# Performance work log

Measured on AMD Instinct MI355X. Metric: run time of the kernel, lower is better.

Reference implementation:

```python
import jax, jax.numpy as jnp
import numpy as np

N, E, D, L, G = 50000, 800000, 96, 3, 256
CD, CH, LAT = 7, 5, 64
BN_EPS = 1e-5


def setup_inputs() -> dict:
    key = jax.random.key(0)
    ks = iter(jax.random.split(key, 32))
    nrm = lambda shape, s=0.1: jax.random.normal(next(ks), shape, dtype=jnp.float32) * s
    return {
        "x": jax.random.normal(next(ks), (N, D), dtype=jnp.float32),
        "cond": jax.random.normal(next(ks), (G, CD), dtype=jnp.float32),
        "edge_index": jax.random.randint(next(ks), (2, E), 0, N),
        "batch": jnp.sort(jax.random.randint(next(ks), (N,), 0, G)),
        "conv_W1": nrm((L, D, D)),
        "conv_b1": nrm((L, D)),
        "conv_g": jnp.ones((L, D), jnp.float32),
        "conv_beta": jnp.zeros((L, D), jnp.float32),
        "conv_mean": jnp.zeros((L, D), jnp.float32),
        "conv_var": jnp.ones((L, D), jnp.float32),
        "conv_W2": nrm((L, D, D)),
        "conv_b2": nrm((L, D)),
        "cW1": nrm((CD, CH)),
        "cb1": nrm((CH,)),
        "cg": jnp.ones((CH,), jnp.float32),
        "cbeta": jnp.zeros((CH,), jnp.float32),
        "cmean": jnp.zeros((CH,), jnp.float32),
        "cvar": jnp.ones((CH,), jnp.float32),
        "cW2": nrm((CH, CH)),
        "cb2": nrm((CH,)),
        "bn_g": jnp.ones((D + CH,), jnp.float32),
        "bn_b": jnp.zeros((D + CH,), jnp.float32),
        "bn_mean": jnp.zeros((D + CH,), jnp.float32),
        "bn_var": jnp.ones((D + CH,), jnp.float32),
        "fc_W": nrm((D + CH, LAT)),
        "fc_b": nrm((LAT,)),
    }


def _bn(h, g, b, mu, var):
    # BatchNorm1d in eval mode: normalize with running stats
    return (h - mu) * (g / jnp.sqrt(var + BN_EPS)) + b


def reference(x, cond, edge_index, batch,
              conv_W1, conv_b1, conv_g, conv_beta, conv_mean, conv_var, conv_W2, conv_b2,
              cW1, cb1, cg, cbeta, cmean, cvar, cW2, cb2,
              bn_g, bn_b, bn_mean, bn_var, fc_W, fc_b):
    src, dst = edge_index[0], edge_index[1]
    n_nodes = x.shape[0]
    h = x
    for l in range(conv_W1.shape[0]):
        # GINConv (eps=0): h_i <- MLP(h_i + sum_{j in N(i)} h_j)
        agg = jax.ops.segment_sum(h[src], dst, num_segments=n_nodes)  # [N, D]
        h = h + agg
        h = jax.nn.leaky_relu(h @ conv_W1[l] + conv_b1[l], 0.2)
        h = _bn(h, conv_g[l], conv_beta[l], conv_mean[l], conv_var[l])
        h = jax.nn.leaky_relu(h @ conv_W2[l] + conv_b2[l], 0.2)
        # dropout is identity in eval mode
    pooled = jax.ops.segment_sum(h, batch, num_segments=cond.shape[0])  # [G, D]
    # conditioning MLP: Linear -> BN -> ReLU -> Linear -> ReLU
    c = cond @ cW1 + cb1
    c = jax.nn.relu(_bn(c, cg, cbeta, cmean, cvar))
    c = jax.nn.relu(c @ cW2 + cb2)
    out = jnp.concatenate([c, pooled], axis=1)  # [G, CH + D]
    out = _bn(out, bn_g, bn_b, bn_mean, bn_var)
    return out @ fc_W + fc_b  # [G, LAT]
```

## Files before the change

### kernel.cpp

```cpp
#include <hip/hip_runtime.h>

#define BN_EPS 1e-5f

__device__ __forceinline__ float lrelu(float x){ return x > 0.f ? x : 0.2f*x; }

struct F3 { float x, y, z; };


__global__ __launch_bounds__(256) void hist_k(const int* __restrict__ dst,
                                              int* __restrict__ deg, int E){
  int e = blockIdx.x*256 + threadIdx.x;
  if (e < E) atomicAdd(&deg[dst[e]], 1);
}

__global__ __launch_bounds__(256) void scan1_k(int* __restrict__ degoff,
                                               int* __restrict__ bsum, int N){
  __shared__ int s[256];
  int t = threadIdx.x, i = blockIdx.x*256 + t;
  int v = (i < N) ? degoff[i] : 0;
  s[t] = v; __syncthreads();
  int x = v;
  for (int d = 1; d < 256; d <<= 1){
    int y = (t >= d) ? s[t-d] : 0;
    __syncthreads();
    x += y; s[t] = x;
    __syncthreads();
  }
  if (i < N) degoff[i] = x - v;
  if (t == 255) bsum[blockIdx.x] = x;
}

__global__ __launch_bounds__(256) void scan2_k(int* __restrict__ bsum, int nb){
  __shared__ int s[256];
  int t = threadIdx.x;
  int v = (t < nb) ? bsum[t] : 0;
  s[t] = v; __syncthreads();
  int x = v;
  for (int d = 1; d < 256; d <<= 1){
    int y = (t >= d) ? s[t-d] : 0;
    __syncthreads();
    x += y; s[t] = x;
    __syncthreads();
  }
  if (t < nb) bsum[t] = x - v;
}

__global__ __launch_bounds__(256) void scan3_k(int* __restrict__ off,
                                               int* __restrict__ cursor,
                                               const int* __restrict__ bsum,
                                               int N, int E){
  int i = blockIdx.x*256 + threadIdx.x;
  if (i < N){
    int o = off[i] + bsum[blockIdx.x];
    off[i] = o; cursor[i] = o;
  }
  if (i == 0) off[N] = E;
}

__global__ __launch_bounds__(256) void scatter_k(const int* __restrict__ src,
                                                 const int* __restrict__ dst,
                                                 int* __restrict__ cursor,
                                                 int* __restrict__ srcs, int E){
  int e = blockIdx.x*256 + threadIdx.x;
  if (e < E){
    int p = atomicAdd(&cursor[dst[e]], 1);
    srcs[p] = src[e];
  }
}

__global__ __launch_bounds__(256) void agg_k(const float* __restrict__ hin,
                                             float* __restrict__ hout,
                                             const int* __restrict__ off,
                                             const int* __restrict__ srcs, int N){
  int node = blockIdx.x*8 + (threadIdx.x >> 5);
  int ln = threadIdx.x & 31;
  if (node >= N) return;
  F3 a = *((const F3*)(hin + (size_t)node*96) + ln);
  float bx = 0.f, by = 0.f, bz = 0.f;
  int jb = off[node], je = off[node+1];
  int j = jb;
  for (; j+1 < je; j += 2){
    int s0 = srcs[j], s1 = srcs[j+1];
    F3 q0 = *((const F3*)(hin + (size_t)s0*96) + ln);
    F3 q1 = *((const F3*)(hin + (size_t)s1*96) + ln);
    a.x += q0.x; a.y += q0.y; a.z += q0.z;
    bx  += q1.x; by  += q1.y; bz  += q1.z;
  }
  if (j < je){
    int s0 = srcs[j];
    F3 q0 = *((const F3*)(hin + (size_t)s0*96) + ln);
    a.x += q0.x; a.y += q0.y; a.z += q0.z;
  }
  a.x += bx; a.y += by; a.z += bz;
  *((F3*)(hout + (size_t)node*96) + ln) = a;
}

__global__ __launch_bounds__(256) void mlp_sw_k(
    const float* __restrict__ hin, float* __restrict__ hout,
    const float* __restrict__ W1, const float* __restrict__ b1,
    const float* __restrict__ g, const float* __restrict__ beta,
    const float* __restrict__ mean, const float* __restrict__ var,
    const float* __restrict__ W2, const float* __restrict__ b2, int N)
{
  __shared__ float hT[96*67];
  int t = threadIdx.x;
  int nbase = blockIdx.x * 64;
  int lim = (N - nbase) * 96;
  const float* hbase = hin + (size_t)nbase*96;

  #pragma unroll
  for (int i = 0; i < 24; ++i){
    int tid = t + 256*i;
    float v = (tid < lim) ? hbase[tid] : 0.f;
    int n = tid / 96, k = tid - n*96;
    hT[k*67 + n] = v;
  }
  __syncthreads();

  int ln = t & 63;
  int d0 = __builtin_amdgcn_readfirstlane((t >> 6) * 24);

  float acc[24];
  #pragma unroll
  for (int j = 0; j < 24; ++j) acc[j] = b1[d0+j];
  #pragma unroll 2
  for (int k = 0; k < 96; ++k){
    float hk = hT[k*67 + ln];
    const float* wr = W1 + k*96 + d0;
    #pragma unroll
    for (int j = 0; j < 24; ++j) acc[j] = fmaf(hk, wr[j], acc[j]);
  }
  __syncthreads();

  #pragma unroll
  for (int j = 0; j < 24; ++j){
    int d = d0 + j;
    float s = g[d] * rsqrtf(var[d] + BN_EPS);
    float m = lrelu(acc[j]);
    hT[d*67 + ln] = (m - mean[d])*s + beta[d];
  }
  __syncthreads();

  #pragma unroll
  for (int j = 0; j < 24; ++j) acc[j] = b2[d0+j];
  #pragma unroll 2
  for (int k = 0; k < 96; ++k){
    float hk = hT[k*67 + ln];
    const float* wr = W2 + k*96 + d0;
    #pragma unroll
    for (int j = 0; j < 24; ++j) acc[j] = fmaf(hk, wr[j], acc[j]);
  }
  __syncthreads();

  #pragma unroll
  for (int j = 0; j < 24; ++j)
    hT[(d0+j)*67 + ln] = lrelu(acc[j]);
  __syncthreads();

  float* obase = hout + (size_t)nbase*96;
  #pragma unroll
  for (int i = 0; i < 24; ++i){
    int tid = t + 256*i;
    int n = tid / 96, k = tid - n*96;
    if (tid < lim) obase[tid] = hT[k*67 + n];
  }
}


__global__ __launch_bounds__(256) void bounds_k(const int* __restrict__ batch,
                                                int* __restrict__ go, int N, int G){
  int i = blockIdx.x*256 + threadIdx.x;
  if (i >= N) return;
  int b = batch[i];
  int prev = (i == 0) ? -1 : batch[i-1];
  for (int g = prev+1; g <= b; ++g) go[g] = i;
  if (i == N-1){
    for (int g = b+1; g <= G; ++g) go[g] = N;
  }
}

__global__ __launch_bounds__(384) void poolfinal_k(
    const float* __restrict__ h, const int* __restrict__ go,
    const float* __restrict__ cond,
    const float* __restrict__ cW1, const float* __restrict__ cb1,
    const float* __restrict__ cg, const float* __restrict__ cbeta,
    const float* __restrict__ cmean, const float* __restrict__ cvar,
    const float* __restrict__ cW2, const float* __restrict__ cb2,
    const float* __restrict__ bn_g, const float* __restrict__ bn_b,
    const float* __restrict__ bn_mean, const float* __restrict__ bn_var,
    const float* __restrict__ fcW, const float* __restrict__ fcb,
    float* __restrict__ out)
{
  __shared__ float ps[4][96];
  __shared__ float pl[96];
  int g = blockIdx.x, t = threadIdx.x;
  int s = t / 96, d = t - s*96;
  {
    float acc = 0.f;
    int nb = go[g], ne = go[g+1];
    for (int n = nb + s; n < ne; n += 4) acc += h[(size_t)n*96 + d];
    ps[s][d] = acc;
  }
  __syncthreads();
  if (t < 96) pl[t] = ps[0][t] + ps[1][t] + ps[2][t] + ps[3][t];
  __syncthreads();

  if (t < 64){
    float cin[7];
    #pragma unroll
    for (int j = 0; j < 7; ++j) cin[j] = cond[g*7+j];
    float c1[5];
    #pragma unroll
    for (int i = 0; i < 5; ++i){
      float a = cb1[i];
      #pragma unroll
      for (int j = 0; j < 7; ++j) a = fmaf(cin[j], cW1[j*5+i], a);
      float sc = cg[i] * rsqrtf(cvar[i] + BN_EPS);
      a = (a - cmean[i])*sc + cbeta[i];
      c1[i] = a > 0.f ? a : 0.f;
    }
    float c2[5];
    #pragma unroll
    for (int i = 0; i < 5; ++i){
      float a = cb2[i];
      #pragma unroll
      for (int j = 0; j < 5; ++j) a = fmaf(c1[j], cW2[j*5+i], a);
      c2[i] = a > 0.f ? a : 0.f;
    }
    float acc = fcb[t];
    #pragma unroll
    for (int j = 0; j < 5; ++j){
      float sc = bn_g[j] * rsqrtf(bn_var[j] + BN_EPS);
      float nb = (c2[j] - bn_mean[j])*sc + bn_b[j];
      acc = fmaf(nb, fcW[j*64 + t], acc);
    }
    for (int j = 5; j < 101; ++j){
      float vj = pl[j-5];
      float sc = bn_g[j] * rsqrtf(bn_var[j] + BN_EPS);
      float nb = (vj - bn_mean[j])*sc + bn_b[j];
      acc = fmaf(nb, fcW[j*64 + t], acc);
    }
    out[g*64 + t] = acc;
  }
}


extern "C" void kernel_launch(void* const* d_in, const int* in_sizes, int n_in,
                              void* d_out, int out_size, void* d_ws, size_t ws_size,
                              hipStream_t stream)
{
  const float* x         = (const float*)d_in[0];
  const float* cond      = (const float*)d_in[1];
  const int*   ei        = (const int*)  d_in[2];
  const int*   batch     = (const int*)  d_in[3];
  const float* conv_W1   = (const float*)d_in[4];
  const float* conv_b1   = (const float*)d_in[5];
  const float* conv_g    = (const float*)d_in[6];
  const float* conv_beta = (const float*)d_in[7];
  const float* conv_mean = (const float*)d_in[8];
  const float* conv_var  = (const float*)d_in[9];
  const float* conv_W2   = (const float*)d_in[10];
  const float* conv_b2   = (const float*)d_in[11];
  const float* cW1       = (const float*)d_in[12];
  const float* cb1       = (const float*)d_in[13];
  const float* cg        = (const float*)d_in[14];
  const float* cbeta     = (const float*)d_in[15];
  const float* cmean     = (const float*)d_in[16];
  const float* cvar      = (const float*)d_in[17];
  const float* cW2       = (const float*)d_in[18];
  const float* cb2       = (const float*)d_in[19];
  const float* bn_g      = (const float*)d_in[20];
  const float* bn_b      = (const float*)d_in[21];
  const float* bn_mean   = (const float*)d_in[22];
  const float* bn_var    = (const float*)d_in[23];
  const float* fc_W      = (const float*)d_in[24];
  const float* fc_b      = (const float*)d_in[25];

  const int D = 96;
  int N = in_sizes[0] / D;
  int G = in_sizes[1] / 7;
  int E = in_sizes[2] / 2;
  const int* src = ei;
  const int* dst = ei + E;

  char* p = (char*)d_ws;
  auto carve = [&](size_t bytes)->void*{
    void* r = (void*)p; p += (bytes + 255) & ~(size_t)255; return r;
  };
  int*   off    = (int*)  carve((size_t)(N+1)*4);
  int*   cursor = (int*)  carve((size_t)N*4);
  int*   bsum   = (int*)  carve(256*4);
  int*   srcs   = (int*)  carve((size_t)E*4);
  int*   go     = (int*)  carve((size_t)(G+1)*4);
  float* hA     = (float*)carve((size_t)N*D*4);
  float* hB     = (float*)carve((size_t)N*D*4);

  int gE = (E+255)/256, gN = (N+255)/256;

  hipMemsetAsync(off, 0, (size_t)(N+1)*4, stream);
  hist_k   <<<gE, 256, 0, stream>>>(dst, off, E);
  scan1_k  <<<gN, 256, 0, stream>>>(off, bsum, N);
  scan2_k  <<<1,  256, 0, stream>>>(bsum, gN);
  scan3_k  <<<gN, 256, 0, stream>>>(off, cursor, bsum, N, E);
  scatter_k<<<gE, 256, 0, stream>>>(src, dst, cursor, srcs, E);
  bounds_k <<<gN, 256, 0, stream>>>(batch, go, N, G);

  const float* hin = x;
  int nblk = (N+63)/64;
  for (int l = 0; l < 3; ++l){
    agg_k<<<(N+7)/8, 256, 0, stream>>>(hin, hB, off, srcs, N);
    mlp_sw_k<<<nblk, 256, 0, stream>>>(hB, hA,
        conv_W1 + (size_t)l*D*D, conv_b1 + l*D,
        conv_g + l*D, conv_beta + l*D, conv_mean + l*D, conv_var + l*D,
        conv_W2 + (size_t)l*D*D, conv_b2 + l*D, N);
    hin = hA;
  }

  poolfinal_k<<<G, 384, 0, stream>>>(hA, go, cond,
                                     cW1, cb1, cg, cbeta, cmean, cvar,
                                     cW2, cb2, bn_g, bn_b, bn_mean, bn_var,
                                     fc_W, fc_b, (float*)d_out);
}
```

Before: 486.6 us.

## Two-level bucketed CSR build and 512-thread MLP blocks

Replaces the single global-atomic scatter that builds the CSR source list with a two-pass bucket partition. Edges are first grouped into 128-node buckets using shared-memory histograms, then scattered per bucket with LDS atomics, which is meant to cut contended global atomics and random writes. It adds an 8-byte-per-edge intermediate buffer and several extra launches. Separately, the MLP kernel now runs 512 threads per block, each computing 12 output columns instead of 24, with k-chunked register staging of the LDS reads; this lowers register pressure and raises parallelism per block.

```diff
diff --git a/kernel.cpp b/kernel.cpp
--- a/kernel.cpp
+++ b/kernel.cpp
@@ -46,25 +46,98 @@
 }
 
 __global__ __launch_bounds__(256) void scan3_k(int* __restrict__ off,
-                                               int* __restrict__ cursor,
                                                const int* __restrict__ bsum,
                                                int N, int E){
   int i = blockIdx.x*256 + threadIdx.x;
-  if (i < N){
-    int o = off[i] + bsum[blockIdx.x];
-    off[i] = o; cursor[i] = o;
-  }
+  if (i < N) off[i] += bsum[blockIdx.x];
   if (i == 0) off[N] = E;
 }
 
-__global__ __launch_bounds__(256) void scatter_k(const int* __restrict__ src,
-                                                 const int* __restrict__ dst,
-                                                 int* __restrict__ cursor,
-                                                 int* __restrict__ srcs, int E){
-  int e = blockIdx.x*256 + threadIdx.x;
-  if (e < E){
-    int p = atomicAdd(&cursor[dst[e]], 1);
-    srcs[p] = src[e];
+#define EB 4096
+
+__global__ __launch_bounds__(256) void bhist_k(const int* __restrict__ dst,
+                                               int* __restrict__ bcnt, int E){
+  __shared__ int bh[512];
+  int t = threadIdx.x;
+  bh[t] = 0; bh[t+256] = 0;
+  __syncthreads();
+  int e0 = blockIdx.x*EB;
+  for (int i = 0; i < EB/256; ++i){
+    int e = e0 + i*256 + t;
+    if (e < E) atomicAdd(&bh[dst[e] >> 7], 1);
+  }
+  __syncthreads();
+  if (bh[t])     atomicAdd(&bcnt[t],     bh[t]);
+  if (bh[t+256]) atomicAdd(&bcnt[t+256], bh[t+256]);
+}
+
+__global__ __launch_bounds__(512) void bscan_k(const int* __restrict__ bcnt,
+                                               int* __restrict__ bkt_off,
+                                               int* __restrict__ gcur, int E){
+  __shared__ int s[512];
+  int t = threadIdx.x;
+  int v = bcnt[t];
+  s[t] = v; __syncthreads();
+  int x = v;
+  for (int d = 1; d < 512; d <<= 1){
+    int y = (t >= d) ? s[t-d] : 0;
+    __syncthreads();
+    x += y; s[t] = x;
+    __syncthreads();
+  }
+  bkt_off[t] = x - v;
+  gcur[t]    = x - v;
+  if (t == 511) bkt_off[512] = E;
+}
+
+__global__ __launch_bounds__(256) void bpart_k(const int* __restrict__ src,
+                                               const int* __restrict__ dst,
+                                               int* __restrict__ gcur,
+                                               int2* __restrict__ ebuf, int E){
+  __shared__ int bh[512];
+  __shared__ int base[512];
+  int t = threadIdx.x;
+  bh[t] = 0; bh[t+256] = 0;
+  __syncthreads();
+  int e0 = blockIdx.x*EB;
+  for (int i = 0; i < EB/256; ++i){
+    int e = e0 + i*256 + t;
+    if (e < E) atomicAdd(&bh[dst[e] >> 7], 1);
+  }
+  __syncthreads();
+  #pragma unroll
+  for (int h = 0; h < 2; ++h){
+    int b = t + h*256;
+    base[b] = bh[b] ? atomicAdd(&gcur[b], bh[b]) : 0;
+  }
+  __syncthreads();
+  for (int i = 0; i < EB/256; ++i){
+    int e = e0 + i*256 + t;
+    if (e < E){
+      int s = src[e], d = dst[e];
+      int p = atomicAdd(&base[d >> 7], 1);
+      ebuf[p] = make_int2(s, d);
+    }
+  }
+}
+
+__global__ __launch_bounds__(256) void bscat_k(const int2* __restrict__ ebuf,
+                                               const int* __restrict__ bkt_off,
+                                               const int* __restrict__ off,
+                                               int* __restrict__ srcs, int N){
+  __shared__ int lcur[128];
+  int b = blockIdx.x, t = threadIdx.x;
+  int node_lo = b << 7;
+  if (t < 128){
+    int n = node_lo + t;
+    lcur[t] = (n < N) ? off[n] : 0;
+  }
+  __syncthreads();
+  int eb = bkt_off[b], ee = bkt_off[b+1];
+  for (int e = eb + t; e < ee; e += 256){
+    int2 sd = ebuf[e];
+    int p = atomicAdd(&lcur[sd.y - node_lo], 1);
+    srcs[p] = sd.x;
   }
 }
 
@@ -95,7 +168,7 @@
   *((F3*)(hout + (size_t)node*96) + ln) = a;
 }
 
-__global__ __launch_bounds__(256) void mlp_sw_k(
+__global__ __launch_bounds__(512) void mlp_sw_k(
     const float* __restrict__ hin, float* __restrict__ hout,
     const float* __restrict__ W1, const float* __restrict__ b1,
     const float* __restrict__ g, const float* __restrict__ beta,
@@ -109,8 +182,8 @@
   const float* hbase = hin + (size_t)nbase*96;
 
   #pragma unroll
-  for (int i = 0; i < 24; ++i){
-    int tid = t + 256*i;
+  for (int i = 0; i < 12; ++i){
+    int tid = t + 512*i;
     float v = (tid < lim) ? hbase[tid] : 0.f;
     int n = tid / 96, k = tid - n*96;
     hT[k*67 + n] = v;
@@ -118,22 +191,26 @@
   __syncthreads();
 
   int ln = t & 63;
-  int d0 = __builtin_amdgcn_readfirstlane((t >> 6) * 24);
-
-  float acc[24];
-  #pragma unroll
-  for (int j = 0; j < 24; ++j) acc[j] = b1[d0+j];
-  #pragma unroll 2
-  for (int k = 0; k < 96; ++k){
-    float hk = hT[k*67 + ln];
-    const float* wr = W1 + k*96 + d0;
-    #pragma unroll
-    for (int j = 0; j < 24; ++j) acc[j] = fmaf(hk, wr[j], acc[j]);
-  }
-  __syncthreads();
-
-  #pragma unroll
-  for (int j = 0; j < 24; ++j){
+  int d0 = __builtin_amdgcn_readfirstlane((t >> 6) * 12);
+
+  float acc[12];
+  #pragma unroll
+  for (int j = 0; j < 12; ++j) acc[j] = b1[d0+j];
+  for (int kc = 0; kc < 96; kc += 8){
+    float hc[8];
+    #pragma unroll
+    for (int i = 0; i < 8; ++i) hc[i] = hT[(kc+i)*67 + ln];
+    #pragma unroll
+    for (int i = 0; i < 8; ++i){
+      const float* wr = W1 + (kc+i)*96 + d0;
+      #pragma unroll
+      for (int j = 0; j < 12; ++j) acc[j] = fmaf(hc[i], wr[j], acc[j]);
+    }
+  }
+  __syncthreads();
+
+  #pragma unroll
+  for (int j = 0; j < 12; ++j){
     int d = d0 + j;
     float s = g[d] * rsqrtf(var[d] + BN_EPS);
     float m = lrelu(acc[j]);
@@ -142,25 +219,29 @@
   __syncthreads();
 
   #pragma unroll
-  for (int j = 0; j < 24; ++j) acc[j] = b2[d0+j];
-  #pragma unroll 2
-  for (int k = 0; k < 96; ++k){
-    float hk = hT[k*67 + ln];
-    const float* wr = W2 + k*96 + d0;
-    #pragma unroll
-    for (int j = 0; j < 24; ++j) acc[j] = fmaf(hk, wr[j], acc[j]);
-  }
-  __syncthreads();
-
-  #pragma unroll
-  for (int j = 0; j < 24; ++j)
+  for (int j = 0; j < 12; ++j) acc[j] = b2[d0+j];
+  for (int kc = 0; kc < 96; kc += 8){
+    float hc[8];
+    #pragma unroll
+    for (int i = 0; i < 8; ++i) hc[i] = hT[(kc+i)*67 + ln];
+    #pragma unroll
+    for (int i = 0; i < 8; ++i){
+      const float* wr = W2 + (kc+i)*96 + d0;
+      #pragma unroll
+      for (int j = 0; j < 12; ++j) acc[j] = fmaf(hc[i], wr[j], acc[j]);
+    }
+  }
+  __syncthreads();
+
+  #pragma unroll
+  for (int j = 0; j < 12; ++j)
     hT[(d0+j)*67 + ln] = lrelu(acc[j]);
   __syncthreads();
 
   float* obase = hout + (size_t)nbase*96;
   #pragma unroll
-  for (int i = 0; i < 24; ++i){
-    int tid = t + 256*i;
+  for (int i = 0; i < 12; ++i){
+    int tid = t + 512*i;
     int n = tid / 96, k = tid - n*96;
     if (tid < lim) obase[tid] = hT[k*67 + n];
   }
@@ -287,29 +368,36 @@
   auto carve = [&](size_t bytes)->void*{
     void* r = (void*)p; p += (bytes + 255) & ~(size_t)255; return r;
   };
-  int*   off    = (int*)  carve((size_t)(N+1)*4);
-  int*   cursor = (int*)  carve((size_t)N*4);
-  int*   bsum   = (int*)  carve(256*4);
-  int*   srcs   = (int*)  carve((size_t)E*4);
-  int*   go     = (int*)  carve((size_t)(G+1)*4);
-  float* hA     = (float*)carve((size_t)N*D*4);
-  float* hB     = (float*)carve((size_t)N*D*4);
-
-  int gE = (E+255)/256, gN = (N+255)/256;
-
-  hipMemsetAsync(off, 0, (size_t)(N+1)*4, stream);
-  hist_k   <<<gE, 256, 0, stream>>>(dst, off, E);
-  scan1_k  <<<gN, 256, 0, stream>>>(off, bsum, N);
-  scan2_k  <<<1,  256, 0, stream>>>(bsum, gN);
-  scan3_k  <<<gN, 256, 0, stream>>>(off, cursor, bsum, N, E);
-  scatter_k<<<gE, 256, 0, stream>>>(src, dst, cursor, srcs, E);
-  bounds_k <<<gN, 256, 0, stream>>>(batch, go, N, G);
+  int*   off     = (int*)  carve((size_t)(N+1)*4);
+  int*   bsum    = (int*)  carve(256*4);
+  int*   bcnt    = (int*)  carve(512*4);
+  int*   bkt_off = (int*)  carve(513*4);
+  int*   gcur    = (int*)  carve(512*4);
+  int2*  ebuf    = (int2*) carve((size_t)E*8);
+  int*   srcs    = (int*)  carve((size_t)E*4);
+  int*   go      = (int*)  carve((size_t)(G+1)*4);
+  float* hA      = (float*)carve((size_t)N*D*4);
+  float* hB      = (float*)carve((size_t)N*D*4);
+
+  int gE = (E+255)/256, gN = (N+255)/256, gEB = (E+EB-1)/EB;
+
+  hipMemsetAsync(off,  0, (size_t)(N+1)*4, stream);
+  hipMemsetAsync(bcnt, 0, 512*4, stream);
+  hist_k <<<gE, 256, 0, stream>>>(dst, off, E);
+  scan1_k<<<gN, 256, 0, stream>>>(off, bsum, N);
+  scan2_k<<<1,  256, 0, stream>>>(bsum, gN);
+  scan3_k<<<gN, 256, 0, stream>>>(off, bsum, N, E);
+  bhist_k<<<gEB, 256, 0, stream>>>(dst, bcnt, E);
+  bscan_k<<<1,  512, 0, stream>>>(bcnt, bkt_off, gcur, E);
+  bpart_k<<<gEB, 256, 0, stream>>>(src, dst, gcur, ebuf, E);
+  bscat_k<<<512, 256, 0, stream>>>(ebuf, bkt_off, off, srcs, N);
+  bounds_k<<<gN, 256, 0, stream>>>(batch, go, N, G);
 
   const float* hin = x;
   int nblk = (N+63)/64;
   for (int l = 0; l < 3; ++l){
     agg_k<<<(N+7)/8, 256, 0, stream>>>(hin, hB, off, srcs, N);
-    mlp_sw_k<<<nblk, 256, 0, stream>>>(hB, hA,
+    mlp_sw_k<<<nblk, 512, 0, stream>>>(hB, hA,
         conv_W1 + (size_t)l*D*D, conv_b1 + l*D,
         conv_g + l*D, conv_beta + l*D, conv_mean + l*D, conv_var + l*D,
         conv_W2 + (size_t)l*D*D, conv_b2 + l*D, N);
```

After: 490.6 us. About the same (+0.8%).
